# Kernel tuning notes

Measured on AMD Instinct MI355X. Metric: run time of the kernel, lower is better.

The kernel has to match this reference:

```python
import jax, jax.numpy as jnp
import numpy as np

D_MODEL, N_HEADS, D_FF = 1024, 16, 2752
B, S = 2, 2048
EPS = 1e-5


def setup_inputs() -> dict:
    key = jax.random.key(0)
    ks = jax.random.split(key, 8)
    def w(k, fan_in, fan_out):
        std = np.sqrt(2.0 / (fan_in + fan_out))
        return jax.random.truncated_normal(k, -3.0, 3.0, (fan_in, fan_out), jnp.float32) * std
    return {
        "x": jax.random.normal(ks[0], (B, S, D_MODEL), jnp.float32),
        "g1": jnp.ones((D_MODEL,), jnp.float32),
        "g2": jnp.ones((D_MODEL,), jnp.float32),
        "w_q": w(ks[1], D_MODEL, D_MODEL),
        "w_k": w(ks[2], D_MODEL, D_MODEL),
        "w_v": w(ks[3], D_MODEL, D_MODEL),
        "w_o": w(ks[4], D_MODEL, D_MODEL),
        "w1": w(ks[5], D_MODEL, D_FF),
        "w2": w(ks[6], D_FF, D_MODEL),
        "w3": w(ks[7], D_MODEL, D_FF),
    }


def rmsnorm(x, g):
    xf = x.astype(jnp.float32)
    rms = jnp.sqrt(jnp.mean(xf * xf, axis=-1, keepdims=True) + EPS)
    return (xf / rms).astype(x.dtype) * g


def reference(x, g1, g2, w_q, w_k, w_v, w_o, w1, w2, w3):
    b, s, d = x.shape
    h = N_HEADS
    dh = d // h

    # --- causal multi-head self-attention on norm1(x) ---
    xn = rmsnorm(x, g1)
    q = (xn @ w_q).reshape(b, s, h, dh).transpose(0, 2, 1, 3)  # b h s d
    k = (xn @ w_k).reshape(b, s, h, dh).transpose(0, 2, 1, 3)
    v = (xn @ w_v).reshape(b, s, h, dh).transpose(0, 2, 1, 3)

    scores = jnp.einsum('bhqd,bhkd->bhqk', q, k) / jnp.sqrt(jnp.float32(dh))
    causal = jnp.tril(jnp.ones((s, s), dtype=bool))
    scores = jnp.where(causal, scores, -jnp.inf)
    probs = jax.nn.softmax(scores, axis=-1)
    attn = jnp.einsum('bhqk,bhkd->bhqd', probs, v)
    attn = attn.transpose(0, 2, 1, 3).reshape(b, s, d)
    h_res = x + attn @ w_o

    # --- SwiGLU FFN on norm2(h) ---
    hn = rmsnorm(h_res, g2)
    x1 = hn @ w1
    gate = x1 * jax.nn.sigmoid(x1)
    ffn = (gate * (hn @ w3)) @ w2
    return h_res + ffn
```

## Files before the change

kernel.cpp:

```cpp
#include <hip/hip_runtime.h>
#include <hip/hip_bf16.h>

typedef unsigned short u16;
typedef __bf16 bf16x8 __attribute__((ext_vector_type(8)));
typedef float  f32x4  __attribute__((ext_vector_type(4)));

#define D_MODEL 1024
#define SEQ     2048
#define NHEAD   16
#define DHEAD   64
#define QKVS    3072

__device__ __forceinline__ float bflo(unsigned u) { return __uint_as_float(u << 16); }
__device__ __forceinline__ float bfhi(unsigned u) { return __uint_as_float(u & 0xffff0000u); }
__device__ __forceinline__ u16 f2bf(float f) {
    unsigned u = __float_as_uint(f);
    u += 0x7fffu + ((u >> 16) & 1u);
    return (u16)(u >> 16);
}
__device__ __forceinline__ u16 f2bf_fast(float f) {
    return (u16)((__float_as_uint(f) + 0x8000u) >> 16);
}
__device__ __forceinline__ void gld_lds16(const u16* g, u16* l) {
    __builtin_amdgcn_global_load_lds((const __attribute__((address_space(1))) void*)g,
                                     (__attribute__((address_space(3))) void*)l, 16, 0, 0);
}

__global__ void detect_k(const unsigned* __restrict__ g1w, int* __restrict__ flag) {
    int c = 0;
#pragma unroll
    for (int i = 0; i < 8; ++i) c += (g1w[i] == 0x3F800000u) ? 1 : 0;
    *flag = (c >= 4) ? 1 : 0;
}

__global__ __launch_bounds__(256) void tp_k(const void* __restrict__ in_, u16* __restrict__ out,
                                            int K, int N, const int* __restrict__ flagp) {
    __shared__ u16 tile[32][33];
    const int f32 = *flagp;
    int k0 = blockIdx.x * 32, n0 = blockIdx.y * 32;
    int tx = threadIdx.x & 31, ty = threadIdx.x >> 5;
#pragma unroll
    for (int i = 0; i < 32; i += 8) {
        int nn = n0 + tx;
        u16 v = 0;
        if (nn < N) {
            size_t idx = (size_t)(k0 + ty + i) * N + nn;
            v = f32 ? f2bf(((const float*)in_)[idx]) : ((const u16*)in_)[idx];
        }
        tile[ty + i][tx] = v;
    }
    __syncthreads();
#pragma unroll
    for (int i = 0; i < 32; i += 8)
        out[(size_t)(n0 + ty + i) * K + (k0 + tx)] = tile[tx][ty + i];
}

__global__ __launch_bounds__(256) void tpm_k(const void* __restrict__ a, const void* __restrict__ b,
                                             const void* __restrict__ c, u16* __restrict__ out,
                                             int K, int N, int outStride,
                                             const int* __restrict__ flagp) {
    __shared__ u16 tile[32][33];
    const void* in_ = (blockIdx.z == 0) ? a : (blockIdx.z == 1) ? b : c;
    u16* o = out + (size_t)blockIdx.z * outStride;
    const int f32 = *flagp;
    int k0 = blockIdx.x * 32, n0 = blockIdx.y * 32;
    int tx = threadIdx.x & 31, ty = threadIdx.x >> 5;
#pragma unroll
    for (int i = 0; i < 32; i += 8) {
        int nn = n0 + tx;
        u16 v = 0;
        if (nn < N) {
            size_t idx = (size_t)(k0 + ty + i) * N + nn;
            v = f32 ? f2bf(((const float*)in_)[idx]) : ((const u16*)in_)[idx];
        }
        tile[ty + i][tx] = v;
    }
    __syncthreads();
#pragma unroll
    for (int i = 0; i < 32; i += 8)
        o[(size_t)(n0 + ty + i) * K + (k0 + tx)] = tile[tx][ty + i];
}

__global__ __launch_bounds__(256) void rms_k(const void* __restrict__ x_, const void* __restrict__ g_,
                                             u16* __restrict__ o, const int* __restrict__ flagp,
                                             int x_raw) {
    const size_t row = blockIdx.x;
    const int f32 = *flagp;
    const int xf32 = f32 & x_raw;
    int t = threadIdx.x;
    float f0, f1, f2, f3, g0, g1, g2, g3;
    if (xf32) {
        float4 xv = *(const float4*)((const float*)x_ + row * D_MODEL + t * 4);
        f0 = xv.x; f1 = xv.y; f2 = xv.z; f3 = xv.w;
    } else {
        uint2 u = *(const uint2*)((const u16*)x_ + row * D_MODEL + t * 4);
        f0 = bflo(u.x); f1 = bfhi(u.x); f2 = bflo(u.y); f3 = bfhi(u.y);
    }
    if (f32) {
        float4 gv = *(const float4*)((const float*)g_ + t * 4);
        g0 = gv.x; g1 = gv.y; g2 = gv.z; g3 = gv.w;
    } else {
        uint2 gu = *(const uint2*)((const u16*)g_ + t * 4);
        g0 = bflo(gu.x); g1 = bfhi(gu.x); g2 = bflo(gu.y); g3 = bfhi(gu.y);
    }
    float s = f0 * f0 + f1 * f1 + f2 * f2 + f3 * f3;
#pragma unroll
    for (int off = 32; off > 0; off >>= 1) s += __shfl_xor(s, off, 64);
    __shared__ float ps[4];
    if ((t & 63) == 0) ps[t >> 6] = s;
    __syncthreads();
    float tot = ps[0] + ps[1] + ps[2] + ps[3];
    float rinv = rsqrtf(tot * (1.0f / D_MODEL) + 1e-5f);
    float fv[4] = {f0, f1, f2, f3};
    float gv2[4] = {g0, g1, g2, g3};
    u16 r[4];
#pragma unroll
    for (int i = 0; i < 4; ++i)
        r[i] = f2bf(fv[i] * rinv * gv2[i]);
    uint2 w;
    w.x = (unsigned)r[0] | ((unsigned)r[1] << 16);
    w.y = (unsigned)r[2] | ((unsigned)r[3] << 16);
    *(uint2*)(o + row * D_MODEL + t * 4) = w;
}

__global__ __launch_bounds__(256) void gemm_k(const u16* __restrict__ A, int lda,
                                              const u16* __restrict__ Bt, int ldb,
                                              u16* C, int ldc,
                                              const void* res, int K, int mode,
                                              const int* __restrict__ flagp, int res_raw,
                                              int out32) {
    __shared__ alignas(16) u16 As[128 * 32];
    __shared__ alignas(16) u16 Bs[128 * 32];
    const int t = threadIdx.x;
    const int rf32 = (mode == 1 && res_raw) ? *flagp : 0;
    const int wid = t >> 6, lane = t & 63;
    const int wm = (wid >> 1) * 64, wn = (wid & 1) * 64;
    const int m0 = blockIdx.x * 128, n0 = blockIdx.y * 128;
    const int fr = lane & 15, quad = lane >> 4;

    f32x4 acc[4][4] = {};

    for (int k0 = 0; k0 < K; k0 += 32) {
        __syncthreads();
#pragma unroll
        for (int r = 0; r < 2; ++r) {
            int e = r * 256 + t;
            int row = e >> 2, c = (e & 3) * 8;
            gld_lds16(A  + (size_t)(m0 + row) * lda + k0 + c, As + e * 8);
            gld_lds16(Bt + (size_t)(n0 + row) * ldb + k0 + c, Bs + e * 8);
        }
        __syncthreads();
        bf16x8 af[4], bfr[4];
#pragma unroll
        for (int i = 0; i < 4; ++i) {
            af[i]  = *(const bf16x8*)(As + (wm + i * 16 + fr) * 32 + quad * 8);
            bfr[i] = *(const bf16x8*)(Bs + (wn + i * 16 + fr) * 32 + quad * 8);
        }
#pragma unroll
        for (int i = 0; i < 4; ++i)
#pragma unroll
            for (int j = 0; j < 4; ++j)
                acc[i][j] = __builtin_amdgcn_mfma_f32_16x16x32_bf16(af[i], bfr[j], acc[i][j], 0, 0, 0);
    }

#pragma unroll
    for (int i = 0; i < 4; ++i)
#pragma unroll
        for (int j = 0; j < 4; ++j)
#pragma unroll
            for (int r2 = 0; r2 < 4; ++r2) {
                int row = m0 + wm + i * 16 + quad * 4 + r2;
                int col = n0 + wn + j * 16 + fr;
                size_t idx = (size_t)row * ldc + col;
                float v = acc[i][j][r2];
                if (mode == 1) {
                    float rv = rf32 ? ((const float*)res)[idx]
                                    : __uint_as_float((unsigned)((const u16*)res)[idx] << 16);
                    v += rv;
                }
                if (out32) ((float*)C)[idx] = v;
                else       C[idx] = f2bf(v);
            }
}

__global__ __launch_bounds__(256) void gemm64_k(const u16* __restrict__ A, int lda,
                                                const u16* __restrict__ Bt, int ldb,
                                                u16* C, int ldc,
                                                const void* res, int K, int mode,
                                                const int* __restrict__ flagp, int res_raw,
                                                int out32) {
    __shared__ alignas(16) u16 As[64 * 32];
    __shared__ alignas(16) u16 Bs[128 * 32];
    const int t = threadIdx.x;
    const int rf32 = (mode == 1 && res_raw) ? *flagp : 0;
    const int wid = t >> 6, lane = t & 63;
    const int wm = (wid >> 1) * 32, wn = (wid & 1) * 64;
    const int m0 = blockIdx.x * 64, n0 = blockIdx.y * 128;
    const int fr = lane & 15, quad = lane >> 4;

    f32x4 acc[2][4] = {};

    for (int k0 = 0; k0 < K; k0 += 32) {
        __syncthreads();
        {
            int row = t >> 2, c = (t & 3) * 8;
            gld_lds16(A + (size_t)(m0 + row) * lda + k0 + c, As + t * 8);
        }
#pragma unroll
        for (int r = 0; r < 2; ++r) {
            int e = r * 256 + t;
            int row = e >> 2, c = (e & 3) * 8;
            gld_lds16(Bt + (size_t)(n0 + row) * ldb + k0 + c, Bs + e * 8);
        }
        __syncthreads();
        bf16x8 af[2], bfr[4];
#pragma unroll
        for (int i = 0; i < 2; ++i)
            af[i] = *(const bf16x8*)(As + (wm + i * 16 + fr) * 32 + quad * 8);
#pragma unroll
        for (int j = 0; j < 4; ++j)
            bfr[j] = *(const bf16x8*)(Bs + (wn + j * 16 + fr) * 32 + quad * 8);
#pragma unroll
        for (int i = 0; i < 2; ++i)
#pragma unroll
            for (int j = 0; j < 4; ++j)
                acc[i][j] = __builtin_amdgcn_mfma_f32_16x16x32_bf16(af[i], bfr[j], acc[i][j], 0, 0, 0);
    }

#pragma unroll
    for (int i = 0; i < 2; ++i)
#pragma unroll
        for (int j = 0; j < 4; ++j)
#pragma unroll
            for (int r2 = 0; r2 < 4; ++r2) {
                int row = m0 + wm + i * 16 + quad * 4 + r2;
                int col = n0 + wn + j * 16 + fr;
                size_t idx = (size_t)row * ldc + col;
                float v = acc[i][j][r2];
                if (mode == 1) {
                    float rv = rf32 ? ((const float*)res)[idx]
                                    : __uint_as_float((unsigned)((const u16*)res)[idx] << 16);
                    v += rv;
                }
                if (out32) ((float*)C)[idx] = v;
                else       C[idx] = f2bf(v);
            }
}

__global__ __launch_bounds__(256, 2) void ffn_k(const u16* __restrict__ A,
                                                const u16* __restrict__ B1t,
                                                const u16* __restrict__ B3t,
                                                u16* __restrict__ G, int ldg) {
    __shared__ alignas(16) u16 As[128 * 32];
    __shared__ alignas(16) u16 B1s[128 * 32];
    __shared__ alignas(16) u16 B3s[128 * 32];
    const int t = threadIdx.x;
    const int wid = t >> 6, lane = t & 63;
    const int wm = (wid >> 1) * 64, wn = (wid & 1) * 64;
    const int m0 = blockIdx.x * 128, n0 = blockIdx.y * 128;
    const int fr = lane & 15, quad = lane >> 4;

    f32x4 acc1[4][4] = {};
    f32x4 acc3[4][4] = {};

    for (int k0 = 0; k0 < 1024; k0 += 32) {
        __syncthreads();
#pragma unroll
        for (int r = 0; r < 2; ++r) {
            int e = r * 256 + t;
            int row = e >> 2, c = (e & 3) * 8;
            gld_lds16(A   + (size_t)(m0 + row) * 1024 + k0 + c, As  + e * 8);
            gld_lds16(B1t + (size_t)(n0 + row) * 1024 + k0 + c, B1s + e * 8);
            gld_lds16(B3t + (size_t)(n0 + row) * 1024 + k0 + c, B3s + e * 8);
        }
        __syncthreads();
        bf16x8 af[4], b1[4], b3[4];
#pragma unroll
        for (int i = 0; i < 4; ++i) {
            af[i] = *(const bf16x8*)(As  + (wm + i * 16 + fr) * 32 + quad * 8);
            b1[i] = *(const bf16x8*)(B1s + (wn + i * 16 + fr) * 32 + quad * 8);
            b3[i] = *(const bf16x8*)(B3s + (wn + i * 16 + fr) * 32 + quad * 8);
        }
#pragma unroll
        for (int i = 0; i < 4; ++i)
#pragma unroll
            for (int j = 0; j < 4; ++j) {
                acc1[i][j] = __builtin_amdgcn_mfma_f32_16x16x32_bf16(af[i], b1[j], acc1[i][j], 0, 0, 0);
                acc3[i][j] = __builtin_amdgcn_mfma_f32_16x16x32_bf16(af[i], b3[j], acc3[i][j], 0, 0, 0);
            }
    }

#pragma unroll
    for (int i = 0; i < 4; ++i)
#pragma unroll
        for (int j = 0; j < 4; ++j)
#pragma unroll
            for (int r2 = 0; r2 < 4; ++r2) {
                int row = m0 + wm + i * 16 + quad * 4 + r2;
                int col = n0 + wn + j * 16 + fr;
                float xv = acc1[i][j][r2];
                xv = fminf(fmaxf(xv, -60.f), 60.f);
                float sg = xv / (1.0f + __expf(-xv));
                G[(size_t)row * ldg + col] = f2bf(sg * acc3[i][j][r2]);
            }
}

__global__ __launch_bounds__(256) void vtp_k(const u16* __restrict__ qkv, u16* __restrict__ vt) {
    __shared__ u16 tile[32][33];
    const int bh = blockIdx.z, b = bh >> 4, h = bh & 15;
    const int s0 = blockIdx.x * 32, d0 = blockIdx.y * 32;
    const int tx = threadIdx.x & 31, ty = threadIdx.x >> 5;
#pragma unroll
    for (int i = 0; i < 32; i += 8)
        tile[ty + i][tx] = qkv[(size_t)(b * SEQ + s0 + ty + i) * QKVS + 2048 + h * 64 + d0 + tx];
    __syncthreads();
#pragma unroll
    for (int i = 0; i < 32; i += 8)
        vt[(size_t)(bh * 64 + d0 + ty + i) * SEQ + s0 + tx] = tile[tx][ty + i];
}

#define KPAD 68
#define PPAD 72
__global__ __launch_bounds__(256) void fattn_k(const u16* __restrict__ QKV, const u16* __restrict__ Vt,
                                               u16* __restrict__ O, u16* __restrict__ pO,
                                               float* __restrict__ pL) {
    __shared__ alignas(16) u16 Ks[64 * KPAD];
    __shared__ alignas(16) u16 Vs[64 * KPAD];
    __shared__ alignas(16) u16 Ps[4 * 32 * PPAD];

    const int bh = blockIdx.y;
    const int j = blockIdx.x;
    int chunk, kt0, ktn, partial, slot;
    if (j < 16) {
        chunk = 15 - (j >> 1);
        int h = chunk + 1;
        int half = j & 1;
        kt0 = half * h; ktn = h; partial = 1;
        slot = (bh << 4) + ((chunk - 8) << 1) + half;
    } else {
        chunk = 23 - j; kt0 = 0; ktn = 2 * (chunk + 1); partial = 0; slot = 0;
    }

    const size_t baseqk = ((size_t)(bh >> 4) * SEQ) * QKVS + (size_t)(bh & 15) * DHEAD;
    const size_t baseo  = ((size_t)(bh >> 4) * SEQ) * D_MODEL + (size_t)(bh & 15) * DHEAD;
    const size_t vtbase = (size_t)bh * 64 * SEQ;
    const u16* Qp = QKV + baseqk;
    const u16* Kp = QKV + baseqk + 1024;
    const int r0 = chunk * 128;
    const int t = threadIdx.x, w = t >> 6, lane = t & 63;
    const int fr = lane & 15, quad = lane >> 4;

    bf16x8 qa[2][2];
#pragma unroll
    for (int s = 0; s < 2; ++s) {
        const u16* qp = Qp + (size_t)(r0 + w * 32 + s * 16 + fr) * QKVS + quad * 8;
        qa[s][0] = *(const bf16x8*)(qp);
        qa[s][1] = *(const bf16x8*)(qp + 32);
    }

    f32x4 oacc[2][4] = {};
    float lp[2][4] = {};
    u16* Pw = Ps + w * 32 * PPAD;
    const float sc = 0.125f * 1.44269504f;
    const int qrow_min = r0 + w * 32;

    for (int kt = kt0; kt < kt0 + ktn; ++kt) {
        const int kb = kt * 64;
        __syncthreads();
#pragma unroll
        for (int it = 0; it < 2; ++it) {
            int e = it * 256 + t;
            int rr = e >> 3, cc = (e & 7) * 8;
            *(uint4*)(Ks + rr * KPAD + cc) = *(const uint4*)(Kp + (size_t)(kb + rr) * QKVS + cc);
            *(uint4*)(Vs + rr * KPAD + cc) = *(const uint4*)(Vt + vtbase + (size_t)rr * SEQ + kb + cc);
        }
        __syncthreads();

#pragma unroll
        for (int s = 0; s < 2; ++s) {
            f32x4 sac[4] = {};
#pragma unroll
            for (int n = 0; n < 4; ++n) {
                bf16x8 kf0 = *(const bf16x8*)(Ks + (n * 16 + fr) * KPAD + quad * 8);
                bf16x8 kf1 = *(const bf16x8*)(Ks + (n * 16 + fr) * KPAD + 32 + quad * 8);
                sac[n] = __builtin_amdgcn_mfma_f32_16x16x32_bf16(qa[s][0], kf0, sac[n], 0, 0, 0);
                sac[n] = __builtin_amdgcn_mfma_f32_16x16x32_bf16(qa[s][1], kf1, sac[n], 0, 0, 0);
            }
            const int smin = qrow_min + s * 16;
            if (kb + 64 <= smin) {
#pragma unroll
                for (int n = 0; n < 4; ++n)
#pragma unroll
                    for (int r = 0; r < 4; ++r) {
                        float p = exp2f(fminf(sac[n][r] * sc, 126.f));
                        lp[s][r] += p;
                        Pw[(s * 16 + quad * 4 + r) * PPAD + n * 16 + fr] = f2bf_fast(p);
                    }
            } else {
                const int qb_s = smin + quad * 4;
#pragma unroll
                for (int n = 0; n < 4; ++n) {
                    int key = kb + n * 16 + fr;
#pragma unroll
                    for (int r = 0; r < 4; ++r) {
                        float p = (key <= qb_s + r) ? exp2f(fminf(sac[n][r] * sc, 126.f)) : 0.f;
                        lp[s][r] += p;
                        Pw[(s * 16 + quad * 4 + r) * PPAD + n * 16 + fr] = f2bf_fast(p);
                    }
                }
            }
        }
        __threadfence_block();
        bf16x8 vf0[4], vf1[4];
#pragma unroll
        for (int n = 0; n < 4; ++n) {
            vf0[n] = *(const bf16x8*)(Vs + (n * 16 + fr) * KPAD + quad * 8);
            vf1[n] = *(const bf16x8*)(Vs + (n * 16 + fr) * KPAD + 32 + quad * 8);
        }
#pragma unroll
        for (int s = 0; s < 2; ++s) {
            bf16x8 pa0 = *(const bf16x8*)(Pw + (s * 16 + fr) * PPAD + quad * 8);
            bf16x8 pa1 = *(const bf16x8*)(Pw + (s * 16 + fr) * PPAD + 32 + quad * 8);
#pragma unroll
            for (int n = 0; n < 4; ++n) {
                oacc[s][n] = __builtin_amdgcn_mfma_f32_16x16x32_bf16(pa0, vf0[n], oacc[s][n], 0, 0, 0);
                oacc[s][n] = __builtin_amdgcn_mfma_f32_16x16x32_bf16(pa1, vf1[n], oacc[s][n], 0, 0, 0);
            }
        }
    }

#pragma unroll
    for (int s = 0; s < 2; ++s)
#pragma unroll
        for (int r = 0; r < 4; ++r) {
            float v = lp[s][r];
            v += __shfl_xor(v, 1, 64);
            v += __shfl_xor(v, 2, 64);
            v += __shfl_xor(v, 4, 64);
            v += __shfl_xor(v, 8, 64);
            lp[s][r] = v;
        }
    if (!partial) {
#pragma unroll
        for (int s = 0; s < 2; ++s)
#pragma unroll
            for (int r = 0; r < 4; ++r) {
                float linv = 1.0f / lp[s][r];
                u16* op = O + baseo + (size_t)(qrow_min + s * 16 + quad * 4 + r) * D_MODEL;
#pragma unroll
                for (int n = 0; n < 4; ++n)
                    op[n * 16 + fr] = f2bf(oacc[s][n][r] * linv);
            }
    } else {
        u16* po = pO + (size_t)slot * 8192;
#pragma unroll
        for (int s = 0; s < 2; ++s)
#pragma unroll
            for (int r = 0; r < 4; ++r) {
                int rl = w * 32 + s * 16 + quad * 4 + r;
#pragma unroll
                for (int n = 0; n < 4; ++n)
                    po[rl * 64 + n * 16 + fr] = f2bf(oacc[s][n][r]);
                if (fr == 0) pL[slot * 128 + rl] = lp[s][r];
            }
    }
}

__global__ __launch_bounds__(256) void fcomb_k(const u16* __restrict__ pO, const float* __restrict__ pL,
                                               u16* __restrict__ O) {
    const int id = blockIdx.x;
    const int bh = id >> 3, chunk = 8 + (id & 7);
    const int s0 = (bh << 4) + ((chunk - 8) << 1);
    const size_t baseo = ((size_t)(bh >> 4) * SEQ) * D_MODEL + (size_t)(bh & 15) * DHEAD;
    const int r0 = chunk * 128;
    const u16* p0 = pO + (size_t)s0 * 8192;
    const u16* p1 = p0 + 8192;
    for (int e = threadIdx.x; e < 8192; e += 256) {
        int row = e >> 6, d = e & 63;
        float o = __uint_as_float((unsigned)p0[e] << 16) + __uint_as_float((unsigned)p1[e] << 16);
        float l = pL[s0 * 128 + row] + pL[(s0 + 1) * 128 + row];
        O[baseo + (size_t)(r0 + row) * D_MODEL + d] = f2bf(o / l);
    }
}

extern "C" void kernel_launch(void* const* d_in, const int* in_sizes, int n_in,
                              void* d_out, int out_size, void* d_ws, size_t ws_size,
                              hipStream_t stream) {
    const void* x  = d_in[0];
    const void* g1 = d_in[1];
    const void* g2 = d_in[2];
    const void* wq = d_in[3];
    const void* wk = d_in[4];
    const void* wv = d_in[5];
    const void* wo = d_in[6];
    const void* w1 = d_in[7];
    const void* w2 = d_in[8];
    const void* w3 = d_in[9];
    u16* ws  = (u16*)d_ws;

    u16*   xn    = ws;
    float* pL    = (float*)ws;
    u16*   qkv   = ws + 4194304;
    u16*   gate  = ws + 4194304;
    u16*   pO    = ws + 16777216;
    u16*   hres  = ws + 16777216;
    int*   flag  = (int*)(ws + 20971520);
    u16*   wqkvT = ws + 20971776;
    u16*   woT   = ws + 20971776;
    u16*   w2T   = ws + 20971776;
    u16*   vt    = (u16*)d_out;
    u16*   attn  = (u16*)d_out + 4194304;
    u16*   w1T   = (u16*)d_out;
    u16*   w3T   = (u16*)d_out + 2883584;

    detect_k<<<1, 1, 0, stream>>>((const unsigned*)g1, flag);

    tpm_k<<<dim3(32, 32, 3), 256, 0, stream>>>(wq, wk, wv, wqkvT, 1024, 1024, 1048576, flag);
    rms_k<<<4096, 256, 0, stream>>>(x, g1, xn, flag, 1);

    gemm_k<<<dim3(32, 24), 256, 0, stream>>>(xn, 1024, wqkvT, 1024, qkv, QKVS, nullptr, 1024, 0, flag, 0, 0);

    tp_k<<<dim3(32, 32), 256, 0, stream>>>(wo, woT, 1024, 1024, flag);
    vtp_k<<<dim3(64, 2, 32), 256, 0, stream>>>(qkv, vt);
    fattn_k<<<dim3(24, 32), 256, 0, stream>>>(qkv, vt, attn, pO, pL);
    fcomb_k<<<256, 256, 0, stream>>>(pO, pL, attn);

    gemm64_k<<<dim3(64, 8), 256, 0, stream>>>(attn, 1024, woT, 1024, hres, 1024, x, 1024, 1, flag, 1, 0);

    rms_k<<<4096, 256, 0, stream>>>(hres, g2, xn, flag, 0);

    tpm_k<<<dim3(32, 88, 2), 256, 0, stream>>>(w1, w3, w3, w1T, 1024, 2752, 2883584, flag);
    tp_k<<<dim3(86, 32), 256, 0, stream>>>(w2, w2T, 2752, 1024, flag);

    ffn_k<<<dim3(32, 22), 256, 0, stream>>>(xn, w1T, w3T, gate, 2816);

    gemm64_k<<<dim3(64, 8), 256, 0, stream>>>(gate, 2816, w2T, 2752, (u16*)d_out, 1024, hres, 2752, 1, flag, 0, 1);
}
```

Measured before the change: 437.0 us.

## Double-buffer K/V tiles in flash attention with register prefetch and MFMA priority

The attention kernel now keeps two LDS buffers for the K and V tiles. It issues the global loads for the next tile into registers before computing the current one and writes them to the alternate buffer afterwards, so each iteration needs one barrier instead of two. It also raises wave priority around the MFMA blocks with s_setprio. The aim is to hide global-load latency behind matrix work, at the cost of doubled LDS for K/V, extra registers, and possibly lower occupancy.

```diff
diff --git a/kernel.cpp b/kernel.cpp
--- a/kernel.cpp
+++ b/kernel.cpp
@@ -324,8 +324,8 @@
 __global__ __launch_bounds__(256) void fattn_k(const u16* __restrict__ QKV, const u16* __restrict__ Vt,
                                                u16* __restrict__ O, u16* __restrict__ pO,
                                                float* __restrict__ pL) {
-    __shared__ alignas(16) u16 Ks[64 * KPAD];
-    __shared__ alignas(16) u16 Vs[64 * KPAD];
+    __shared__ alignas(16) u16 Ks[2][64 * KPAD];
+    __shared__ alignas(16) u16 Vs[2][64 * KPAD];
     __shared__ alignas(16) u16 Ps[4 * 32 * PPAD];
 
     const int bh = blockIdx.y;
@@ -350,6 +350,8 @@
     const int t = threadIdx.x, w = t >> 6, lane = t & 63;
     const int fr = lane & 15, quad = lane >> 4;
 
+    const int rr = t >> 3, cc = (t & 7) * 8;
+
     bf16x8 qa[2][2];
 #pragma unroll
     for (int s = 0; s < 2; ++s) {
@@ -364,28 +366,43 @@
     const float sc = 0.125f * 1.44269504f;
     const int qrow_min = r0 + w * 32;
 
+    uint4 kreg0, kreg1, vreg0, vreg1;
+#define LOADT(kt_) do { int kb_ = (kt_) * 64;                                              \
+        kreg0 = *(const uint4*)(Kp + (size_t)(kb_ + rr) * QKVS + cc);                      \
+        kreg1 = *(const uint4*)(Kp + (size_t)(kb_ + 32 + rr) * QKVS + cc);                 \
+        vreg0 = *(const uint4*)(Vt + vtbase + (size_t)rr * SEQ + kb_ + cc);                \
+        vreg1 = *(const uint4*)(Vt + vtbase + (size_t)(32 + rr) * SEQ + kb_ + cc); } while (0)
+#define WRITET(b_) do {                                                                    \
+        *(uint4*)(Ks[b_] + rr * KPAD + cc)        = kreg0;                                 \
+        *(uint4*)(Ks[b_] + (32 + rr) * KPAD + cc) = kreg1;                                 \
+        *(uint4*)(Vs[b_] + rr * KPAD + cc)        = vreg0;                                 \
+        *(uint4*)(Vs[b_] + (32 + rr) * KPAD + cc) = vreg1; } while (0)
+
+    LOADT(kt0);
+    WRITET(0);
+    __syncthreads();
+    int cur = 0;
+
     for (int kt = kt0; kt < kt0 + ktn; ++kt) {
         const int kb = kt * 64;
-        __syncthreads();
-#pragma unroll
-        for (int it = 0; it < 2; ++it) {
-            int e = it * 256 + t;
-            int rr = e >> 3, cc = (e & 7) * 8;
-            *(uint4*)(Ks + rr * KPAD + cc) = *(const uint4*)(Kp + (size_t)(kb + rr) * QKVS + cc);
-            *(uint4*)(Vs + rr * KPAD + cc) = *(const uint4*)(Vt + vtbase + (size_t)rr * SEQ + kb + cc);
-        }
-        __syncthreads();
+        const int have = (kt + 1 < kt0 + ktn);
+        if (have) LOADT(kt + 1);
+
+        const u16* Kc = Ks[cur];
+        const u16* Vc = Vs[cur];
 
 #pragma unroll
         for (int s = 0; s < 2; ++s) {
             f32x4 sac[4] = {};
+            __builtin_amdgcn_s_setprio(1);
 #pragma unroll
             for (int n = 0; n < 4; ++n) {
-                bf16x8 kf0 = *(const bf16x8*)(Ks + (n * 16 + fr) * KPAD + quad * 8);
-                bf16x8 kf1 = *(const bf16x8*)(Ks + (n * 16 + fr) * KPAD + 32 + quad * 8);
+                bf16x8 kf0 = *(const bf16x8*)(Kc + (n * 16 + fr) * KPAD + quad * 8);
+                bf16x8 kf1 = *(const bf16x8*)(Kc + (n * 16 + fr) * KPAD + 32 + quad * 8);
                 sac[n] = __builtin_amdgcn_mfma_f32_16x16x32_bf16(qa[s][0], kf0, sac[n], 0, 0, 0);
                 sac[n] = __builtin_amdgcn_mfma_f32_16x16x32_bf16(qa[s][1], kf1, sac[n], 0, 0, 0);
             }
+            __builtin_amdgcn_s_setprio(0);
             const int smin = qrow_min + s * 16;
             if (kb + 64 <= smin) {
 #pragma unroll
@@ -414,9 +431,10 @@
         bf16x8 vf0[4], vf1[4];
 #pragma unroll
         for (int n = 0; n < 4; ++n) {
-            vf0[n] = *(const bf16x8*)(Vs + (n * 16 + fr) * KPAD + quad * 8);
-            vf1[n] = *(const bf16x8*)(Vs + (n * 16 + fr) * KPAD + 32 + quad * 8);
-        }
+            vf0[n] = *(const bf16x8*)(Vc + (n * 16 + fr) * KPAD + quad * 8);
+            vf1[n] = *(const bf16x8*)(Vc + (n * 16 + fr) * KPAD + 32 + quad * 8);
+        }
+        __builtin_amdgcn_s_setprio(1);
 #pragma unroll
         for (int s = 0; s < 2; ++s) {
             bf16x8 pa0 = *(const bf16x8*)(Pw + (s * 16 + fr) * PPAD + quad * 8);
@@ -427,7 +445,14 @@
                 oacc[s][n] = __builtin_amdgcn_mfma_f32_16x16x32_bf16(pa1, vf1[n], oacc[s][n], 0, 0, 0);
             }
         }
-    }
+        __builtin_amdgcn_s_setprio(0);
+
+        if (have) WRITET(cur ^ 1);
+        __syncthreads();
+        cur ^= 1;
+    }
+#undef LOADT
+#undef WRITET
 
 #pragma unroll
     for (int s = 0; s < 2; ++s)
```

Measured after the change: 498.5 us. 1.14x slower.

## Rebalance causal flash-attention work with table-driven split-K partitioning

Applied to the files above, without the earlier changes.

Replaces the fixed two-way split of the long query chunks with a constant lookup table that splits chunks 6-15 into 2-4 key-range pieces, so the 38 blocks per head carry roughly equal work (6-8 key tiles each). The combine kernel now merges a variable number of partials per chunk. Partial buffers are spread across two workspace regions and pL is moved to its own area. This is meant to cut tail imbalance in the causal attention grid, at the cost of more partial writes and combine traffic.

```diff
diff --git a/kernel.cpp b/kernel.cpp
--- a/kernel.cpp
+++ b/kernel.cpp
@@ -321,8 +321,18 @@
 
 #define KPAD 68
 #define PPAD 72
+__constant__ int JC[38]  = {5,4, 15,15,15,15, 11,11,11, 7,7, 14,14, 10, 3, 14,14,
+                            13,13,13,13, 12,12, 10,10, 9,9, 6,6, 12,12, 9, 8,8,8, 2, 1, 0};
+__constant__ int JK0[38] = {0,0, 0,8,16,24, 0,8,16, 0,8, 7,22, 14, 0, 0,15,
+                            0,7,14,21, 6,19, 0,7, 6,13, 0,7, 0,13, 0, 0,6,12, 0, 0, 0};
+__constant__ int JKN[38] = {12,10, 8,8,8,8, 8,8,8, 8,8, 8,8, 8, 8, 7,7,
+                            7,7,7,7, 7,7, 7,7, 7,7, 7,7, 6,6, 6, 6,6,6, 6, 4, 2};
+__constant__ int JSL[38] = {-1,-1, 28,29,30,31, 13,14,15, 2,3, 25,27, 12, -1, 24,26,
+                            20,21,22,23, 17,19, 10,11, 8,9, 0,1, 16,18, 7, 4,5,6, -1, -1, -1};
+
 __global__ __launch_bounds__(256) void fattn_k(const u16* __restrict__ QKV, const u16* __restrict__ Vt,
-                                               u16* __restrict__ O, u16* __restrict__ pO,
+                                               u16* __restrict__ O,
+                                               u16* __restrict__ pOa, u16* __restrict__ pOb,
                                                float* __restrict__ pL) {
     __shared__ alignas(16) u16 Ks[64 * KPAD];
     __shared__ alignas(16) u16 Vs[64 * KPAD];
@@ -330,16 +340,9 @@
 
     const int bh = blockIdx.y;
     const int j = blockIdx.x;
-    int chunk, kt0, ktn, partial, slot;
-    if (j < 16) {
-        chunk = 15 - (j >> 1);
-        int h = chunk + 1;
-        int half = j & 1;
-        kt0 = half * h; ktn = h; partial = 1;
-        slot = (bh << 4) + ((chunk - 8) << 1) + half;
-    } else {
-        chunk = 23 - j; kt0 = 0; ktn = 2 * (chunk + 1); partial = 0; slot = 0;
-    }
+    const int chunk = JC[j], kt0 = JK0[j], ktn = JKN[j], sl = JSL[j];
+    const int partial = (sl >= 0);
+    const int slot = bh * 32 + sl;
 
     const size_t baseqk = ((size_t)(bh >> 4) * SEQ) * QKVS + (size_t)(bh & 15) * DHEAD;
     const size_t baseo  = ((size_t)(bh >> 4) * SEQ) * D_MODEL + (size_t)(bh & 15) * DHEAD;
@@ -452,7 +455,8 @@
                     op[n * 16 + fr] = f2bf(oacc[s][n][r] * linv);
             }
     } else {
-        u16* po = pO + (size_t)slot * 8192;
+        u16* po = (slot < 512) ? (pOa + (size_t)slot * 8192)
+                               : (pOb + (size_t)(slot - 512) * 8192);
 #pragma unroll
         for (int s = 0; s < 2; ++s)
 #pragma unroll
@@ -466,19 +470,28 @@
     }
 }
 
-__global__ __launch_bounds__(256) void fcomb_k(const u16* __restrict__ pO, const float* __restrict__ pL,
+__global__ __launch_bounds__(256) void fcomb_k(const u16* __restrict__ pOa, const u16* __restrict__ pOb,
+                                               const float* __restrict__ pL,
                                                u16* __restrict__ O) {
     const int id = blockIdx.x;
-    const int bh = id >> 3, chunk = 8 + (id & 7);
-    const int s0 = (bh << 4) + ((chunk - 8) << 1);
+    const int bh = id / 10, pc = id % 10;
+    const int chunk = 6 + pc;
+    const int np = 2 + (pc >= 2) + (pc >= 6);
+    const int pref = 2 * (pc < 2 ? pc : 2) + 3 * (pc < 2 ? 0 : (pc < 6 ? pc - 2 : 4))
+                   + 4 * (pc < 6 ? 0 : pc - 6);
+    const int base = bh * 32 + pref;
     const size_t baseo = ((size_t)(bh >> 4) * SEQ) * D_MODEL + (size_t)(bh & 15) * DHEAD;
     const int r0 = chunk * 128;
-    const u16* p0 = pO + (size_t)s0 * 8192;
-    const u16* p1 = p0 + 8192;
     for (int e = threadIdx.x; e < 8192; e += 256) {
         int row = e >> 6, d = e & 63;
-        float o = __uint_as_float((unsigned)p0[e] << 16) + __uint_as_float((unsigned)p1[e] << 16);
-        float l = pL[s0 * 128 + row] + pL[(s0 + 1) * 128 + row];
+        float o = 0.f, l = 0.f;
+        for (int p = 0; p < np; ++p) {
+            int S = base + p;
+            const u16* ptr = (S < 512) ? (pOa + (size_t)S * 8192)
+                                       : (pOb + (size_t)(S - 512) * 8192);
+            o += __uint_as_float((unsigned)ptr[e] << 16);
+            l += pL[S * 128 + row];
+        }
         O[baseo + (size_t)(r0 + row) * D_MODEL + d] = f2bf(o / l);
     }
 }
@@ -499,15 +512,16 @@
     u16* ws  = (u16*)d_ws;
 
     u16*   xn    = ws;
-    float* pL    = (float*)ws;
+    u16*   pOb   = ws;
     u16*   qkv   = ws + 4194304;
     u16*   gate  = ws + 4194304;
-    u16*   pO    = ws + 16777216;
+    u16*   pOa   = ws + 16777216;
     u16*   hres  = ws + 16777216;
     int*   flag  = (int*)(ws + 20971520);
     u16*   wqkvT = ws + 20971776;
     u16*   woT   = ws + 20971776;
     u16*   w2T   = ws + 20971776;
+    float* pL    = (float*)(ws + 23789824);
     u16*   vt    = (u16*)d_out;
     u16*   attn  = (u16*)d_out + 4194304;
     u16*   w1T   = (u16*)d_out;
@@ -522,8 +536,8 @@
 
     tp_k<<<dim3(32, 32), 256, 0, stream>>>(wo, woT, 1024, 1024, flag);
     vtp_k<<<dim3(64, 2, 32), 256, 0, stream>>>(qkv, vt);
-    fattn_k<<<dim3(24, 32), 256, 0, stream>>>(qkv, vt, attn, pO, pL);
-    fcomb_k<<<256, 256, 0, stream>>>(pO, pL, attn);
+    fattn_k<<<dim3(38, 32), 256, 0, stream>>>(qkv, vt, attn, pOa, pOb, pL);
+    fcomb_k<<<320, 256, 0, stream>>>(pOa, pOb, pL, attn);
 
     gemm64_k<<<dim3(64, 8), 256, 0, stream>>>(attn, 1024, woT, 1024, hres, 1024, x, 1024, 1, flag, 1, 0);
 
```

After: 457.4 us. +4.7%, slower.
